# Optimization experiments

Hardware: AMD Instinct MI355X
Metric: run time of the kernel (lower is better)

Reference implementation:

```python
import jax, jax.numpy as jnp
import numpy as np

M, IN, H, OUT, B = 64, 64, 256, 1, 4096


def setup_inputs() -> dict:
    key = jax.random.key(0)
    ks = jax.random.split(key, 7)
    s1 = 1.0 / np.sqrt(IN)
    s2 = 1.0 / np.sqrt(H)
    return {
        "xs": jax.random.normal(ks[0], (M, B, IN), dtype=jnp.float32),
        "W1": jax.random.uniform(ks[1], (M, IN, H), minval=-s1, maxval=s1, dtype=jnp.float32),
        "b1": jax.random.uniform(ks[2], (M, H), minval=-s1, maxval=s1, dtype=jnp.float32),
        "W2": jax.random.uniform(ks[3], (M, H, H), minval=-s2, maxval=s2, dtype=jnp.float32),
        "b2": jax.random.uniform(ks[4], (M, H), minval=-s2, maxval=s2, dtype=jnp.float32),
        "W3": jax.random.uniform(ks[5], (M, H, OUT), minval=-s2, maxval=s2, dtype=jnp.float32),
        "b3": jax.random.uniform(ks[6], (M, OUT), minval=-s2, maxval=s2, dtype=jnp.float32),
    }


def reference(xs, W1, b1, W2, b2, W3, b3):
    # Batched over models: [M, B, in] x [M, in, h] -> [M, B, h]
    h1 = jax.nn.relu(jnp.einsum("mbi,mih->mbh", xs, W1) + b1[:, None, :])
    h2 = jax.nn.relu(jnp.einsum("mbh,mhk->mbk", h1, W2) + b2[:, None, :])
    out = jnp.einsum("mbh,mho->mbo", h2, W3) + b3[:, None, :]
    return out  # [M, B, out]
```

## Files before the change

### kernel.cpp

```cpp
#include <hip/hip_runtime.h>

#define NMODELS 64
#define BBATCH  4096
#define IN_DIM  64
#define H_DIM   256

typedef __attribute__((ext_vector_type(8))) short short8;
typedef __attribute__((ext_vector_type(4))) float floatx4;

__device__ __forceinline__ unsigned short f2bf(float f) {
    unsigned int u = __builtin_bit_cast(unsigned int, f);
    u += 0x7FFFu + ((u >> 16) & 1u);
    return (unsigned short)(u >> 16);
}

__global__ __launch_bounds__(256) void transpose_cvt(const float* __restrict__ src,
                                                     unsigned short* __restrict__ dst,
                                                     int K, int N) {
    __shared__ float lds[64 * 65];
    const int kt = K >> 6, nt = N >> 6;
    const int t = blockIdx.x;
    const int m = t / (kt * nt);
    const int rem = t - m * (kt * nt);
    const int kb = rem / nt, nb = rem - kb * nt;
    const int tid = threadIdx.x;
    const int c = tid & 63, rq = tid >> 6;

    const float* s = src + ((size_t)m * K + (size_t)kb * 64) * N + nb * 64;
#pragma unroll
    for (int it = 0; it < 16; ++it) {
        int r = it * 4 + rq;
        lds[c * 65 + r] = s[(size_t)r * N + c];
    }
    __syncthreads();
    unsigned short* d = dst + ((size_t)m * N + (size_t)nb * 64) * K + kb * 64;
#pragma unroll
    for (int it = 0; it < 16; ++it) {
        int n = it * 4 + rq;
        d[(size_t)n * K + c] = f2bf(lds[n * 65 + c]);
    }
}

__global__ __launch_bounds__(256, 2) void mlp_fused(
    const float* __restrict__ xs,
    const unsigned short* __restrict__ w1t,
    const float* __restrict__ b1,
    const unsigned short* __restrict__ w2t,
    const float* __restrict__ b2,
    const float* __restrict__ w3,
    const float* __restrict__ b3,
    float* __restrict__ out)
{
    __shared__ unsigned short h1s[64 * 256];
    __shared__ float red[4][64];

    const int bid = blockIdx.x;
    const int m   = bid >> 6;
    const int tb  = bid & 63;
    const int tid = threadIdx.x;
    const int w   = tid >> 6;
    const int lane = tid & 63;
    const int q   = lane >> 4;
    const int c16 = lane & 15;
    const int sw  = c16 & 7;

    const float* xrow = xs + ((size_t)m * BBATCH + (size_t)tb * 64) * IN_DIM;
    const unsigned short* w1p = w1t + (size_t)m * (H_DIM * IN_DIM)
                                + (w * 64 + c16) * IN_DIM + q * 8;

    short8 ax[4][2];
#pragma unroll
    for (int rb = 0; rb < 4; ++rb)
#pragma unroll
        for (int kb = 0; kb < 2; ++kb) {
            const float* xp = xrow + (rb * 16 + c16) * IN_DIM + kb * 32 + q * 8;
            float4 v0 = *(const float4*)xp;
            float4 v1 = *(const float4*)(xp + 4);
            short8 a;
            a[0] = (short)f2bf(v0.x); a[1] = (short)f2bf(v0.y);
            a[2] = (short)f2bf(v0.z); a[3] = (short)f2bf(v0.w);
            a[4] = (short)f2bf(v1.x); a[5] = (short)f2bf(v1.y);
            a[6] = (short)f2bf(v1.z); a[7] = (short)f2bf(v1.w);
            ax[rb][kb] = a;
        }

    floatx4 acc[4][4];
#pragma unroll
    for (int rb = 0; rb < 4; ++rb)
#pragma unroll
        for (int nb = 0; nb < 4; ++nb)
            acc[rb][nb] = (floatx4){0.f, 0.f, 0.f, 0.f};

#pragma unroll
    for (int kb = 0; kb < 2; ++kb) {
        short8 bw[4];
#pragma unroll
        for (int nb = 0; nb < 4; ++nb)
            bw[nb] = *(const short8*)(w1p + nb * (16 * IN_DIM) + kb * 32);
#pragma unroll
        for (int nb = 0; nb < 4; ++nb)
#pragma unroll
            for (int rb = 0; rb < 4; ++rb)
                acc[rb][nb] = __builtin_amdgcn_mfma_f32_16x16x32_bf16(
                    ax[rb][kb], bw[nb], acc[rb][nb], 0, 0, 0);
    }

    const int ncol = w * 64 + c16;
    {
        float b1v[4];
#pragma unroll
        for (int nb = 0; nb < 4; ++nb) b1v[nb] = b1[m * H_DIM + ncol + nb * 16];
#pragma unroll
        for (int rb = 0; rb < 4; ++rb)
#pragma unroll
            for (int nb = 0; nb < 4; ++nb)
#pragma unroll
                for (int r = 0; r < 4; ++r) {
                    float v = fmaxf(acc[rb][nb][r] + b1v[nb], 0.f);
                    int row = rb * 16 + q * 4 + r;
                    int col = ncol + nb * 16;
                    int phys = row * 256 + ((((col >> 3) ^ (row & 7)) << 3) | (col & 7));
                    h1s[phys] = f2bf(v);
                }
    }
    __syncthreads();

#pragma unroll
    for (int rb = 0; rb < 4; ++rb)
#pragma unroll
        for (int nb = 0; nb < 4; ++nb)
            acc[rb][nb] = (floatx4){0.f, 0.f, 0.f, 0.f};

    const unsigned short* w2p = w2t + (size_t)m * (H_DIM * H_DIM)
                                + (w * 64 + c16) * H_DIM + q * 8;
#pragma unroll
    for (int kb = 0; kb < 8; ++kb) {
        short8 av[4], bv[4];
#pragma unroll
        for (int rb = 0; rb < 4; ++rb)
            av[rb] = *(const short8*)&h1s[(rb * 16 + c16) * 256 + (((kb * 4 + q) ^ sw) << 3)];
#pragma unroll
        for (int nb = 0; nb < 4; ++nb)
            bv[nb] = *(const short8*)(w2p + nb * (16 * H_DIM) + kb * 32);
#pragma unroll
        for (int nb = 0; nb < 4; ++nb)
#pragma unroll
            for (int rb = 0; rb < 4; ++rb)
                acc[rb][nb] = __builtin_amdgcn_mfma_f32_16x16x32_bf16(
                    av[rb], bv[nb], acc[rb][nb], 0, 0, 0);
    }

    float b2v[4], w3v[4];
#pragma unroll
    for (int nb = 0; nb < 4; ++nb) {
        b2v[nb] = b2[m * H_DIM + ncol + nb * 16];
        w3v[nb] = w3[m * H_DIM + ncol + nb * 16];
    }
    float p[4][4];
#pragma unroll
    for (int rb = 0; rb < 4; ++rb)
#pragma unroll
        for (int r = 0; r < 4; ++r) p[rb][r] = 0.f;
#pragma unroll
    for (int rb = 0; rb < 4; ++rb)
#pragma unroll
        for (int nb = 0; nb < 4; ++nb)
#pragma unroll
            for (int r = 0; r < 4; ++r) {
                float v = fmaxf(acc[rb][nb][r] + b2v[nb], 0.f);
                p[rb][r] += v * w3v[nb];
            }
#pragma unroll
    for (int off = 1; off < 16; off <<= 1)
#pragma unroll
        for (int rb = 0; rb < 4; ++rb)
#pragma unroll
            for (int r = 0; r < 4; ++r)
                p[rb][r] += __shfl_xor(p[rb][r], off);

    if (c16 == 0) {
#pragma unroll
        for (int rb = 0; rb < 4; ++rb)
#pragma unroll
            for (int r = 0; r < 4; ++r)
                red[w][rb * 16 + q * 4 + r] = p[rb][r];
    }
    __syncthreads();
    if (tid < 64) {
        float s = red[0][tid] + red[1][tid] + red[2][tid] + red[3][tid] + b3[m];
        out[(size_t)m * BBATCH + tb * 64 + tid] = s;
    }
}

extern "C" void kernel_launch(void* const* d_in, const int* in_sizes, int n_in,
                              void* d_out, int out_size, void* d_ws, size_t ws_size,
                              hipStream_t stream) {
    const float* xs = (const float*)d_in[0];
    const float* W1 = (const float*)d_in[1];
    const float* b1 = (const float*)d_in[2];
    const float* W2 = (const float*)d_in[3];
    const float* b2 = (const float*)d_in[4];
    const float* W3 = (const float*)d_in[5];
    const float* b3 = (const float*)d_in[6];
    float* out = (float*)d_out;

    unsigned short* w1t = (unsigned short*)d_ws;
    unsigned short* w2t = w1t + (size_t)NMODELS * H_DIM * IN_DIM;

    transpose_cvt<<<NMODELS * 1 * 4, 256, 0, stream>>>(W1, w1t, IN_DIM, H_DIM);
    transpose_cvt<<<NMODELS * 4 * 4, 256, 0, stream>>>(W2, w2t, H_DIM, H_DIM);
    mlp_fused<<<NMODELS * (BBATCH / 64), 256, 0, stream>>>(xs, w1t, b1, w2t, b2, W3, b3, out);
}
```

Before: 215.2 us.

## Merge weight prep kernels, vectorize stores, remap columns, raise occupancy

The two transpose-and-convert launches become one prep kernel that does vectorized float4 reads and 16-byte bf16 stores. In the fused MLP, each lane now owns 4 contiguous output columns, so bias and W3 loads become float4 and the h1 LDS writes become 8-byte vector stores instead of scalar 2-byte stores. The reduction buffer now reuses the h1 shared memory, guarded by an extra barrier, and launch bounds go from 2 to 4 blocks per SM for more occupancy. Rounding changes to round-half-up instead of round-to-nearest-even, and the extra barrier plus the higher occupancy target could add register pressure.

```diff
diff --git a/kernel.cpp b/kernel.cpp
--- a/kernel.cpp
+++ b/kernel.cpp
@@ -6,42 +6,52 @@
 #define H_DIM   256
 
 typedef __attribute__((ext_vector_type(8))) short short8;
+typedef __attribute__((ext_vector_type(4))) short short4v;
 typedef __attribute__((ext_vector_type(4))) float floatx4;
 
 __device__ __forceinline__ unsigned short f2bf(float f) {
     unsigned int u = __builtin_bit_cast(unsigned int, f);
-    u += 0x7FFFu + ((u >> 16) & 1u);
-    return (unsigned short)(u >> 16);
-}
-
-__global__ __launch_bounds__(256) void transpose_cvt(const float* __restrict__ src,
-                                                     unsigned short* __restrict__ dst,
-                                                     int K, int N) {
-    __shared__ float lds[64 * 65];
-    const int kt = K >> 6, nt = N >> 6;
-    const int t = blockIdx.x;
-    const int m = t / (kt * nt);
-    const int rem = t - m * (kt * nt);
-    const int kb = rem / nt, nb = rem - kb * nt;
+    return (unsigned short)((u + 0x8000u) >> 16);
+}
+
+__global__ __launch_bounds__(256) void prep_weights(const float* __restrict__ W1,
+                                                    const float* __restrict__ W2,
+                                                    unsigned short* __restrict__ w1t,
+                                                    unsigned short* __restrict__ w2t) {
+    __shared__ float lds[64][65];
+    const int bid = blockIdx.x;
+    const float* src;
+    unsigned short* dst;
+    int K, N, m, kb, nb;
+    if (bid < 256) {
+        m = bid >> 2; kb = 0; nb = bid & 3; K = IN_DIM; N = H_DIM;
+        src = W1; dst = w1t;
+    } else {
+        int t = bid - 256;
+        m = t >> 4; kb = (t >> 2) & 3; nb = t & 3; K = H_DIM; N = H_DIM;
+        src = W2; dst = w2t;
+    }
+    const float* s = src + ((size_t)m * K + (size_t)kb * 64) * N + nb * 64;
     const int tid = threadIdx.x;
-    const int c = tid & 63, rq = tid >> 6;
-
-    const float* s = src + ((size_t)m * K + (size_t)kb * 64) * N + nb * 64;
-#pragma unroll
-    for (int it = 0; it < 16; ++it) {
-        int r = it * 4 + rq;
-        lds[c * 65 + r] = s[(size_t)r * N + c];
-    }
-    __syncthreads();
-    unsigned short* d = dst + ((size_t)m * N + (size_t)nb * 64) * K + kb * 64;
-#pragma unroll
-    for (int it = 0; it < 16; ++it) {
-        int n = it * 4 + rq;
-        d[(size_t)n * K + c] = f2bf(lds[n * 65 + c]);
-    }
-}
-
-__global__ __launch_bounds__(256, 2) void mlp_fused(
+    const int r = tid >> 4, c4 = (tid & 15) * 4;
+#pragma unroll
+    for (int p = 0; p < 4; ++p) {
+        int row = p * 16 + r;
+        float4 v = *(const float4*)(s + (size_t)row * N + c4);
+        lds[row][c4] = v.x; lds[row][c4 + 1] = v.y;
+        lds[row][c4 + 2] = v.z; lds[row][c4 + 3] = v.w;
+    }
+    __syncthreads();
+    const int n = tid & 63, kg = tid >> 6;
+    unsigned short tmp[16];
+#pragma unroll
+    for (int j = 0; j < 16; ++j) tmp[j] = f2bf(lds[kg * 16 + j][n]);
+    unsigned short* d = dst + ((size_t)m * N + (size_t)(nb * 64 + n)) * K + kb * 64 + kg * 16;
+    *(short8*)d = *(const short8*)tmp;
+    *(short8*)(d + 8) = *(const short8*)(tmp + 8);
+}
+
+__global__ __launch_bounds__(256, 4) void mlp_fused(
     const float* __restrict__ xs,
     const unsigned short* __restrict__ w1t,
     const float* __restrict__ b1,
@@ -52,7 +62,7 @@
     float* __restrict__ out)
 {
     __shared__ unsigned short h1s[64 * 256];
-    __shared__ float red[4][64];
+    float* red = (float*)h1s;
 
     const int bid = blockIdx.x;
     const int m   = bid >> 6;
@@ -66,7 +76,7 @@
 
     const float* xrow = xs + ((size_t)m * BBATCH + (size_t)tb * 64) * IN_DIM;
     const unsigned short* w1p = w1t + (size_t)m * (H_DIM * IN_DIM)
-                                + (w * 64 + c16) * IN_DIM + q * 8;
+                                + (w * 64 + c16 * 4) * IN_DIM + q * 8;
 
     short8 ax[4][2];
 #pragma unroll
@@ -96,7 +106,7 @@
         short8 bw[4];
 #pragma unroll
         for (int nb = 0; nb < 4; ++nb)
-            bw[nb] = *(const short8*)(w1p + nb * (16 * IN_DIM) + kb * 32);
+            bw[nb] = *(const short8*)(w1p + nb * IN_DIM + kb * 32);
 #pragma unroll
         for (int nb = 0; nb < 4; ++nb)
 #pragma unroll
@@ -105,23 +115,20 @@
                     ax[rb][kb], bw[nb], acc[rb][nb], 0, 0, 0);
     }
 
-    const int ncol = w * 64 + c16;
     {
-        float b1v[4];
-#pragma unroll
-        for (int nb = 0; nb < 4; ++nb) b1v[nb] = b1[m * H_DIM + ncol + nb * 16];
-#pragma unroll
-        for (int rb = 0; rb < 4; ++rb)
-#pragma unroll
-            for (int nb = 0; nb < 4; ++nb)
-#pragma unroll
-                for (int r = 0; r < 4; ++r) {
-                    float v = fmaxf(acc[rb][nb][r] + b1v[nb], 0.f);
-                    int row = rb * 16 + q * 4 + r;
-                    int col = ncol + nb * 16;
-                    int phys = row * 256 + ((((col >> 3) ^ (row & 7)) << 3) | (col & 7));
-                    h1s[phys] = f2bf(v);
-                }
+        floatx4 b1v = *(const floatx4*)(b1 + m * H_DIM + w * 64 + c16 * 4);
+#pragma unroll
+        for (int rb = 0; rb < 4; ++rb)
+#pragma unroll
+            for (int r = 0; r < 4; ++r) {
+                short4v t;
+#pragma unroll
+                for (int nb = 0; nb < 4; ++nb)
+                    t[nb] = (short)f2bf(fmaxf(acc[rb][nb][r] + b1v[nb], 0.f));
+                int row = rb * 16 + q * 4 + r;
+                int chunk = (w * 8 + (c16 >> 1)) ^ (row & 7);
+                *(short4v*)((char*)h1s + row * 512 + chunk * 16 + (c16 & 1) * 8) = t;
+            }
     }
     __syncthreads();
 
@@ -132,16 +139,17 @@
             acc[rb][nb] = (floatx4){0.f, 0.f, 0.f, 0.f};
 
     const unsigned short* w2p = w2t + (size_t)m * (H_DIM * H_DIM)
-                                + (w * 64 + c16) * H_DIM + q * 8;
+                                + (w * 64 + c16 * 4) * H_DIM + q * 8;
 #pragma unroll
     for (int kb = 0; kb < 8; ++kb) {
         short8 av[4], bv[4];
 #pragma unroll
         for (int rb = 0; rb < 4; ++rb)
-            av[rb] = *(const short8*)&h1s[(rb * 16 + c16) * 256 + (((kb * 4 + q) ^ sw) << 3)];
-#pragma unroll
-        for (int nb = 0; nb < 4; ++nb)
-            bv[nb] = *(const short8*)(w2p + nb * (16 * H_DIM) + kb * 32);
+            av[rb] = *(const short8*)((char*)h1s + (rb * 16 + c16) * 512
+                                      + (((kb * 4 + q) ^ sw) * 16));
+#pragma unroll
+        for (int nb = 0; nb < 4; ++nb)
+            bv[nb] = *(const short8*)(w2p + nb * H_DIM + kb * 32);
 #pragma unroll
         for (int nb = 0; nb < 4; ++nb)
 #pragma unroll
@@ -150,12 +158,8 @@
                     av[rb], bv[nb], acc[rb][nb], 0, 0, 0);
     }
 
-    float b2v[4], w3v[4];
-#pragma unroll
-    for (int nb = 0; nb < 4; ++nb) {
-        b2v[nb] = b2[m * H_DIM + ncol + nb * 16];
-        w3v[nb] = w3[m * H_DIM + ncol + nb * 16];
-    }
+    floatx4 b2v = *(const floatx4*)(b2 + m * H_DIM + w * 64 + c16 * 4);
+    floatx4 w3v = *(const floatx4*)(w3 + m * H_DIM + w * 64 + c16 * 4);
     float p[4][4];
 #pragma unroll
     for (int rb = 0; rb < 4; ++rb)
@@ -178,16 +182,17 @@
             for (int r = 0; r < 4; ++r)
                 p[rb][r] += __shfl_xor(p[rb][r], off);
 
+    __syncthreads();
     if (c16 == 0) {
 #pragma unroll
         for (int rb = 0; rb < 4; ++rb)
 #pragma unroll
             for (int r = 0; r < 4; ++r)
-                red[w][rb * 16 + q * 4 + r] = p[rb][r];
+                red[w * 64 + rb * 16 + q * 4 + r] = p[rb][r];
     }
     __syncthreads();
     if (tid < 64) {
-        float s = red[0][tid] + red[1][tid] + red[2][tid] + red[3][tid] + b3[m];
+        float s = red[tid] + red[64 + tid] + red[128 + tid] + red[192 + tid] + b3[m];
         out[(size_t)m * BBATCH + tb * 64 + tid] = s;
     }
 }
@@ -207,7 +212,6 @@
     unsigned short* w1t = (unsigned short*)d_ws;
     unsigned short* w2t = w1t + (size_t)NMODELS * H_DIM * IN_DIM;
 
-    transpose_cvt<<<NMODELS * 1 * 4, 256, 0, stream>>>(W1, w1t, IN_DIM, H_DIM);
-    transpose_cvt<<<NMODELS * 4 * 4, 256, 0, stream>>>(W2, w2t, H_DIM, H_DIM);
+    prep_weights<<<256 + NMODELS * 16, 256, 0, stream>>>(W1, W2, w1t, w2t);
     mlp_fused<<<NMODELS * (BBATCH / 64), 256, 0, stream>>>(xs, w1t, b1, w2t, b2, W3, b3, out);
 }
```

After: 208.5 us. 3.1% less time.
